# Kernel tuning notes

Measured on AMD Instinct MI355X. Metric: run time of the kernel, lower is better.

Reference implementation:

```python
import jax, jax.numpy as jnp
import numpy as np

DIM = 1024
N_HEADS = 16
HEAD_DIM = DIM // N_HEADS
WINDOW = 64


def setup_inputs() -> dict:
    key = jax.random.key(0)
    k1, k2, k3 = jax.random.split(key, 3)
    B, N = 4, 8192
    x = jax.random.normal(k1, (B, N, DIM), dtype=jnp.float32)
    w_qkv = jax.random.normal(k2, (3 * DIM, DIM), dtype=jnp.float32) * (1.0 / np.sqrt(DIM))
    b_qkv = jnp.zeros((3 * DIM,), dtype=jnp.float32)
    w_proj = jax.random.normal(k3, (DIM, DIM), dtype=jnp.float32) * (1.0 / np.sqrt(DIM))
    b_proj = jnp.zeros((DIM,), dtype=jnp.float32)
    return {"x": x, "w_qkv": w_qkv, "b_qkv": b_qkv, "w_proj": w_proj, "b_proj": b_proj}


def reference(x, w_qkv, b_qkv, w_proj, b_proj):
    B, N, C = x.shape
    H, D, W = N_HEADS, HEAD_DIM, WINDOW
    # qkv projection: torch Linear => x @ W.T + b
    qkv = x @ w_qkv.T + b_qkv                      # [B, N, 3C]
    qkv = qkv.reshape(B, N, 3, H, D).transpose(2, 0, 3, 1, 4)  # [3, B, H, N, D]
    q, k, v = qkv[0], qkv[1], qkv[2]               # each [B, H, N, D]
    n_w = N // W                                    # N chosen divisible by window
    # split sequence into non-overlapping windows (block-diagonal attention)
    qw = q.reshape(B, H, n_w, W, D)
    kw = k.reshape(B, H, n_w, W, D)
    vw = v.reshape(B, H, n_w, W, D)
    scale = 1.0 / np.sqrt(D)
    attn = jnp.einsum('bhnqd,bhnkd->bhnqk', qw, kw) * scale  # [B,H,n_w,W,W]
    attn = jax.nn.softmax(attn, axis=-1)
    out = jnp.einsum('bhnqk,bhnkd->bhnqd', attn, vw)          # [B,H,n_w,W,D]
    out = out.reshape(B, H, N, D).transpose(0, 2, 1, 3).reshape(B, N, C)
    return out @ w_proj.T + b_proj
```

## Files before the change

kernel.cpp:

```cpp
#include <hip/hip_runtime.h>
#include <hip/hip_bf16.h>
#include <cstdint>
#include <cstddef>


typedef __attribute__((ext_vector_type(8))) short short8;
typedef __attribute__((ext_vector_type(4))) float float4v;

static __device__ __forceinline__ void async16(void* lds_p, const void* g) {
  __builtin_amdgcn_global_load_lds((const __attribute__((address_space(1))) void*)g,
                                   (__attribute__((address_space(3))) void*)lds_p,
                                   16, 0, 0);
}

static __device__ __forceinline__ unsigned short f2bf_bits(float x) {
  unsigned int u = __float_as_uint(x);
  unsigned int r = (u + 0x7fffu + ((u >> 16) & 1u)) >> 16;
  return (unsigned short)r;
}

#define S_BARRIER() asm volatile("s_barrier" ::: "memory")
#define WAIT_VM(n)  asm volatile("s_waitcnt vmcnt(" #n ")" ::: "memory")
#define WAIT_LGKM0() asm volatile("s_waitcnt lgkmcnt(0)" ::: "memory")

__global__ __launch_bounds__(256) void cast_f32_to_bf16(
    const float* __restrict__ in, unsigned short* __restrict__ out, int n4) {
  int i = blockIdx.x * 256 + threadIdx.x;
  if (i >= n4) return;
  float4 v = ((const float4*)in)[i];
  ushort4 o;
  o.x = f2bf_bits(v.x); o.y = f2bf_bits(v.y);
  o.z = f2bf_bits(v.z); o.w = f2bf_bits(v.w);
  ((ushort4*)out)[i] = o;
}

template<bool OUT_BF16>
__global__ __launch_bounds__(512, 2) void gemm256(
    const unsigned short* __restrict__ A,
    const unsigned short* __restrict__ B,
    const float* __restrict__ bias,
    void* __restrict__ Cout,
    int M, int N, int K, int ntiles)
{
  extern __shared__ unsigned short lds[];

  const int t    = threadIdx.x;
  const int wave = t >> 6;
  const int lane = t & 63;
  const int lr   = lane & 15;
  const int lq   = lane >> 4;
  const int wm   = wave >> 2;
  const int wn   = wave & 3;

  const int nwg  = gridDim.x;
  const int q8   = nwg >> 3;
  const int wg   = ((int)blockIdx.x & 7) * q8 + ((int)blockIdx.x >> 3);
  const int GM   = 8;
  const int group = wg / (GM * ntiles);
  const int inG   = wg % (GM * ntiles);
  const int bm    = group * GM + (inG % GM);
  const int bn    = inG / GM;

  const int srow = t >> 3;
  const int sswz = ((t & 7) ^ (srow & 7)) << 3;
  const unsigned short* Abase = A + (size_t)(bm * 256 + srow) * K + sswz;
  const unsigned short* Bbase = B + (size_t)(bn * 256 + srow) * K + sswz;
  const int ldsw = wave * 512;

  auto stageA = [&](int kt, int c) {
    async16(lds + (kt & 1) * 16384 + c * 4096 + ldsw,
            Abase + (size_t)(c * 64) * K + kt * 64);
  };
  auto stageB = [&](int kt, int c) {
    async16(lds + 32768 + (kt & 1) * 16384 + c * 4096 + ldsw,
            Bbase + (size_t)(c * 64) * K + kt * 64);
  };

  const int g0 = ((0 + lq) ^ (lr & 7)) << 3;
  const int g1 = ((4 + lq) ^ (lr & 7)) << 3;
  const int arow0 = (wm * 128 + lr) * 64;
  const int brow0 = (wn * 64 + lr) * 64;

  float4v acc[8][4];
  #pragma unroll
  for (int i = 0; i < 8; ++i)
    #pragma unroll
    for (int j = 0; j < 4; ++j) acc[i][j] = (float4v){0.f, 0.f, 0.f, 0.f};

  const int NT = K >> 6;

  #pragma unroll
  for (int c = 0; c < 4; ++c) stageB(0, c);
  #pragma unroll
  for (int c = 0; c < 4; ++c) stageA(0, c);
  #pragma unroll
  for (int c = 0; c < 4; ++c) stageB(1, c);
  WAIT_VM(4);
  S_BARRIER();

  short8 af[4][2], bf[2][2], bf2[2][2];

  for (int kt = 0; kt < NT; ++kt) {
    const int bc = kt & 1;
    int kt1 = kt + 1; if (kt1 == NT) kt1 = 0;
    int kt2 = kt + 2; if (kt2 >= NT) kt2 -= NT;
    const unsigned short* Al = lds + bc * 16384;
    const unsigned short* Bl = lds + 32768 + bc * 16384;

    #pragma unroll
    for (int mf = 0; mf < 4; ++mf) {
      af[mf][0] = *(const short8*)(Al + arow0 + mf * 1024 + g0);
      af[mf][1] = *(const short8*)(Al + arow0 + mf * 1024 + g1);
    }
    #pragma unroll
    for (int nf = 0; nf < 2; ++nf) {
      bf[nf][0] = *(const short8*)(Bl + brow0 + nf * 1024 + g0);
      bf[nf][1] = *(const short8*)(Bl + brow0 + nf * 1024 + g1);
    }
    stageA(kt1, 0); stageA(kt1, 2);
    S_BARRIER();
    __builtin_amdgcn_s_setprio(1);
    #pragma unroll
    for (int mf = 0; mf < 4; ++mf)
      #pragma unroll
      for (int nf = 0; nf < 2; ++nf) {
        acc[mf][nf] = __builtin_amdgcn_mfma_f32_16x16x32_bf16(af[mf][0], bf[nf][0], acc[mf][nf], 0, 0, 0);
        acc[mf][nf] = __builtin_amdgcn_mfma_f32_16x16x32_bf16(af[mf][1], bf[nf][1], acc[mf][nf], 0, 0, 0);
      }
    __builtin_amdgcn_s_setprio(0);
    S_BARRIER();

    #pragma unroll
    for (int nf = 0; nf < 2; ++nf) {
      bf2[nf][0] = *(const short8*)(Bl + brow0 + (2 + nf) * 1024 + g0);
      bf2[nf][1] = *(const short8*)(Bl + brow0 + (2 + nf) * 1024 + g1);
    }
    stageA(kt1, 1); stageA(kt1, 3);
    S_BARRIER();
    __builtin_amdgcn_s_setprio(1);
    #pragma unroll
    for (int mf = 0; mf < 4; ++mf)
      #pragma unroll
      for (int nf = 0; nf < 2; ++nf) {
        acc[mf][2 + nf] = __builtin_amdgcn_mfma_f32_16x16x32_bf16(af[mf][0], bf2[nf][0], acc[mf][2 + nf], 0, 0, 0);
        acc[mf][2 + nf] = __builtin_amdgcn_mfma_f32_16x16x32_bf16(af[mf][1], bf2[nf][1], acc[mf][2 + nf], 0, 0, 0);
      }
    __builtin_amdgcn_s_setprio(0);
    S_BARRIER();

    #pragma unroll
    for (int mf = 0; mf < 4; ++mf) {
      af[mf][0] = *(const short8*)(Al + arow0 + (4 + mf) * 1024 + g0);
      af[mf][1] = *(const short8*)(Al + arow0 + (4 + mf) * 1024 + g1);
    }
    stageB(kt2, 0); stageB(kt2, 1);
    S_BARRIER();
    __builtin_amdgcn_s_setprio(1);
    #pragma unroll
    for (int mf = 0; mf < 4; ++mf)
      #pragma unroll
      for (int nf = 0; nf < 2; ++nf) {
        acc[4 + mf][nf] = __builtin_amdgcn_mfma_f32_16x16x32_bf16(af[mf][0], bf[nf][0], acc[4 + mf][nf], 0, 0, 0);
        acc[4 + mf][nf] = __builtin_amdgcn_mfma_f32_16x16x32_bf16(af[mf][1], bf[nf][1], acc[4 + mf][nf], 0, 0, 0);
      }
    __builtin_amdgcn_s_setprio(0);
    S_BARRIER();

    stageB(kt2, 2); stageB(kt2, 3);
    WAIT_VM(4);
    S_BARRIER();
    __builtin_amdgcn_s_setprio(1);
    #pragma unroll
    for (int mf = 0; mf < 4; ++mf)
      #pragma unroll
      for (int nf = 0; nf < 2; ++nf) {
        acc[4 + mf][2 + nf] = __builtin_amdgcn_mfma_f32_16x16x32_bf16(af[mf][0], bf2[nf][0], acc[4 + mf][2 + nf], 0, 0, 0);
        acc[4 + mf][2 + nf] = __builtin_amdgcn_mfma_f32_16x16x32_bf16(af[mf][1], bf2[nf][1], acc[4 + mf][2 + nf], 0, 0, 0);
      }
    __builtin_amdgcn_s_setprio(0);
    S_BARRIER();
  }

  WAIT_VM(0);

  if (OUT_BF16) {
    unsigned short* Ost = lds + wave * 4096;
    const int cb = bn * 256 + wn * 64;
    #pragma unroll
    for (int p = 0; p < 2; ++p) {
      #pragma unroll
      for (int nf = 0; nf < 4; ++nf) {
        const float bv = bias[cb + nf * 16 + lr];
        #pragma unroll
        for (int mh = 0; mh < 4; ++mh)
          #pragma unroll
          for (int r = 0; r < 4; ++r) {
            const int row = mh * 16 + lq * 4 + r;
            Ost[row * 64 + ((nf * 16 + lr) ^ (lq << 4))] =
                f2bf_bits(acc[p * 4 + mh][nf][r] + bv);
          }
      }
      #pragma unroll
      for (int k = 0; k < 8; ++k) {
        const int cid = k * 64 + lane;
        const int row = cid >> 3;
        const int c8  = cid & 7;
        const int lqr = (row >> 2) & 3;
        short8 v = *(const short8*)(Ost + row * 64 + ((c8 * 8) ^ (lqr << 4)));
        const size_t grow = (size_t)(bm * 256 + wm * 128 + p * 64 + row);
        *(short8*)((unsigned short*)Cout + grow * N + cb + c8 * 8) = v;
      }
    }
  } else {
    const int rbase = bm * 256 + wm * 128 + lq * 4;
    const int cbase = bn * 256 + wn * 64 + lr;
    #pragma unroll
    for (int nf = 0; nf < 4; ++nf) {
      const int col = cbase + nf * 16;
      const float bv = bias[col];
      #pragma unroll
      for (int mf = 0; mf < 8; ++mf) {
        const int row = rbase + mf * 16;
        #pragma unroll
        for (int r = 0; r < 4; ++r)
          ((float*)Cout)[(size_t)(row + r) * N + col] = acc[mf][nf][r] + bv;
      }
    }
  }
}

#define WPB 4

__global__ __launch_bounds__(256, 4) void win_attn(
    const unsigned short* __restrict__ qkv,
    unsigned short* __restrict__ out)
{
  __shared__ unsigned short Vt[2][64 * 64];
  __shared__ unsigned short Ps[4 * 16 * 64];

  const int t    = threadIdx.x;
  const int wave = t >> 6;
  const int lane = t & 63;
  const int lr   = lane & 15;
  const int lq   = lane >> 4;
  const int k7   = lane & 7;
  const int kh   = lane >> 3;
  const int gbase = blockIdx.x * WPB;
  unsigned short* Pst = Ps + wave * 1024;

  short8 qa[2], kf[4][2], vr[2];

  auto qptr = [&](int g) {
    const int b = g >> 11, h = (g >> 7) & 15, wi = g & 127;
    return qkv + (size_t)(b * 8192 + wi * 64) * 3072 + h * 64;
  };
  auto loadV = [&](const unsigned short* vb) {
    #pragma unroll
    for (int o = 0; o < 2; ++o)
      vr[o] = *(const short8*)(vb + (size_t)lane * 3072 + wave * 8 + o * 32);
  };
  auto loadQ = [&](const unsigned short* qb) {
    #pragma unroll
    for (int k2 = 0; k2 < 2; ++k2)
      qa[k2] = *(const short8*)(qb + (size_t)(wave * 16 + lr) * 3072 + k2 * 32 + lq * 8);
  };
  auto loadK = [&](const unsigned short* kb) {
    #pragma unroll
    for (int jt = 0; jt < 4; ++jt)
      #pragma unroll
      for (int k2 = 0; k2 < 2; ++k2)
        kf[jt][k2] = *(const short8*)(kb + (size_t)(jt * 16 + lr) * 3072 + k2 * 32 + lq * 8);
  };
  auto scatterV = [&](int s) {
    #pragma unroll
    for (int o = 0; o < 2; ++o) {
      const int d = wave * 8 + o * 32;
      #pragma unroll
      for (int j = 0; j < 8; ++j)
        Vt[s][(d + j) * 64 + k7 + ((kh ^ j) << 3)] = vr[o][j];
    }
  };

  {
    const unsigned short* qb0 = qptr(gbase);
    loadV(qb0 + 2048);
    loadK(qb0 + 1024);
    loadQ(qb0);
    scatterV(0);
    WAIT_LGKM0();
    S_BARRIER();
  }

  for (int i = 0; i < WPB; ++i) {
    const int c = i & 1;
    const int g = gbase + i;
    const int h = (g >> 7) & 15;
    const int tok0 = ((g >> 11) * 8192) + (g & 127) * 64;
    const bool more = (i + 1 < WPB);
    const unsigned short* qb1 = qptr(more ? g + 1 : g);

    if (more) loadV(qb1 + 2048);

    float4v s4[4];
    #pragma unroll
    for (int jt = 0; jt < 4; ++jt) {
      float4v a = (float4v){0.f, 0.f, 0.f, 0.f};
      #pragma unroll
      for (int k2 = 0; k2 < 2; ++k2)
        a = __builtin_amdgcn_mfma_f32_16x16x32_bf16(qa[k2], kf[jt][k2], a, 0, 0, 0);
      s4[jt] = a;
    }

    if (more) { loadK(qb1 + 1024); loadQ(qb1); }

    const float scale = 0.125f;
    float pr[4][4];
    #pragma unroll
    for (int r = 0; r < 4; ++r) {
      float m = s4[0][r];
      #pragma unroll
      for (int jt = 1; jt < 4; ++jt) m = fmaxf(m, s4[jt][r]);
      #pragma unroll
      for (int off = 1; off < 16; off <<= 1) m = fmaxf(m, __shfl_xor(m, off));
      float sum = 0.f;
      #pragma unroll
      for (int jt = 0; jt < 4; ++jt) {
        float e = __expf((s4[jt][r] - m) * scale);
        pr[jt][r] = e; sum += e;
      }
      #pragma unroll
      for (int off = 1; off < 16; off <<= 1) sum += __shfl_xor(sum, off);
      float inv = 1.0f / sum;
      #pragma unroll
      for (int jt = 0; jt < 4; ++jt) pr[jt][r] *= inv;
    }

    #pragma unroll
    for (int jt = 0; jt < 4; ++jt)
      #pragma unroll
      for (int r = 0; r < 4; ++r) {
        const int row = lq * 4 + r;
        const int cu  = (jt * 2 + (lr >> 3)) ^ (row & 7);
        Pst[row * 64 + (cu << 3) + (lr & 7)] = f2bf_bits(pr[jt][r]);
      }
    short8 pa[2];
    #pragma unroll
    for (int k2 = 0; k2 < 2; ++k2)
      pa[k2] = *(const short8*)(&Pst[lr * 64 + (((k2 * 4 + lq) ^ (lr & 7)) << 3)]);

    float4v o4[4];
    #pragma unroll
    for (int jd = 0; jd < 4; ++jd) {
      float4v a = (float4v){0.f, 0.f, 0.f, 0.f};
      #pragma unroll
      for (int k2 = 0; k2 < 2; ++k2) {
        short8 vf = *(const short8*)(&Vt[c][(jd * 16 + lr) * 64 +
                                            (((k2 * 4 + lq) ^ (lr & 7)) << 3)]);
        a = __builtin_amdgcn_mfma_f32_16x16x32_bf16(pa[k2], vf, a, 0, 0, 0);
      }
      o4[jd] = a;
    }

    if (more) scatterV(c ^ 1);

    #pragma unroll
    for (int jd = 0; jd < 4; ++jd)
      #pragma unroll
      for (int r = 0; r < 4; ++r)
        Pst[(lq * 4 + r) * 64 + ((jd * 16 + lr) ^ (lq << 4))] = f2bf_bits(o4[jd][r]);
    #pragma unroll
    for (int k = 0; k < 2; ++k) {
      const int cid = k * 64 + lane;
      const int row = cid >> 3;
      const int c8  = cid & 7;
      const int lqr = (row >> 2) & 3;
      short8 v = *(const short8*)(&Pst[row * 64 + ((c8 * 8) ^ (lqr << 4))]);
      *(short8*)(out + (size_t)(tok0 + wave * 16 + row) * 1024 + h * 64 + c8 * 8) = v;
    }

    if (more) {
      WAIT_LGKM0();
      S_BARRIER();
    }
  }
}

extern "C" void kernel_launch(void* const* d_in, const int* in_sizes, int n_in,
                              void* d_out, int out_size, void* d_ws, size_t ws_size,
                              hipStream_t stream) {
  const float* x      = (const float*)d_in[0];
  const float* w_qkv  = (const float*)d_in[1];
  const float* b_qkv  = (const float*)d_in[2];
  const float* w_proj = (const float*)d_in[3];
  const float* b_proj = (const float*)d_in[4];
  float* outp = (float*)d_out;

  char* ws = (char*)d_ws;
  unsigned short* xb     = (unsigned short*)(ws);
  unsigned short* wqkvb  = (unsigned short*)(ws + 67108864);
  unsigned short* wprojb = (unsigned short*)(ws + 73400320);
  unsigned short* qkvb   = (unsigned short*)(ws + 75497472);
  unsigned short* attnb  = (unsigned short*)(ws + 276824064);

  static int attr_done = 0;
  if (!attr_done) {
    hipFuncSetAttribute(reinterpret_cast<const void*>(&gemm256<true>),
                        hipFuncAttributeMaxDynamicSharedMemorySize, 131072);
    hipFuncSetAttribute(reinterpret_cast<const void*>(&gemm256<false>),
                        hipFuncAttributeMaxDynamicSharedMemorySize, 131072);
    attr_done = 1;
  }

  cast_f32_to_bf16<<<32768, 256, 0, stream>>>(x,      xb,     33554432 / 4);
  cast_f32_to_bf16<<<3072,  256, 0, stream>>>(w_qkv,  wqkvb,  3145728 / 4);
  cast_f32_to_bf16<<<1024,  256, 0, stream>>>(w_proj, wprojb, 1048576 / 4);

  gemm256<true><<<128 * 12, 512, 131072, stream>>>(xb, wqkvb, b_qkv, qkvb,
                                                   32768, 3072, 1024, 12);
  win_attn<<<8192 / WPB, 256, 0, stream>>>(qkvb, attnb);
  gemm256<false><<<128 * 4, 512, 131072, stream>>>(attnb, wprojb, b_proj, outp,
                                                   32768, 1024, 1024, 4);
}
```

Before: 589.9 us.

## Assign one attention window per wave instead of block-shared windows

The windowed attention kernel now gives each wave a whole (batch, head, window) tile. Each wave loads K and V, computes all four 16-row query tiles, and transposes V through its own LDS slice. The block barriers and the cross-wave double-buffered V scatter go away, as does the software prefetch of the next window. In exchange, per-wave LDS use and register pressure rise (pa, vf and vrow are held together), and loads are no longer overlapped with compute across windows.

```diff
diff --git a/kernel.cpp b/kernel.cpp
--- a/kernel.cpp
+++ b/kernel.cpp
@@ -21,7 +21,6 @@
 
 #define S_BARRIER() asm volatile("s_barrier" ::: "memory")
 #define WAIT_VM(n)  asm volatile("s_waitcnt vmcnt(" #n ")" ::: "memory")
-#define WAIT_LGKM0() asm volatile("s_waitcnt lgkmcnt(0)" ::: "memory")
 
 __global__ __launch_bounds__(256) void cast_f32_to_bf16(
     const float* __restrict__ in, unsigned short* __restrict__ out, int n4) {
@@ -229,77 +228,48 @@
   }
 }
 
-#define WPB 4
-
 __global__ __launch_bounds__(256, 4) void win_attn(
     const unsigned short* __restrict__ qkv,
     unsigned short* __restrict__ out)
 {
-  __shared__ unsigned short Vt[2][64 * 64];
-  __shared__ unsigned short Ps[4 * 16 * 64];
+  __shared__ unsigned short Ps[4][64 * 64];
 
   const int t    = threadIdx.x;
   const int wave = t >> 6;
   const int lane = t & 63;
   const int lr   = lane & 15;
   const int lq   = lane >> 4;
+  const int kh   = lane >> 3;
   const int k7   = lane & 7;
-  const int kh   = lane >> 3;
-  const int gbase = blockIdx.x * WPB;
-  unsigned short* Pst = Ps + wave * 1024;
-
-  short8 qa[2], kf[4][2], vr[2];
-
-  auto qptr = [&](int g) {
-    const int b = g >> 11, h = (g >> 7) & 15, wi = g & 127;
-    return qkv + (size_t)(b * 8192 + wi * 64) * 3072 + h * 64;
-  };
-  auto loadV = [&](const unsigned short* vb) {
-    #pragma unroll
-    for (int o = 0; o < 2; ++o)
-      vr[o] = *(const short8*)(vb + (size_t)lane * 3072 + wave * 8 + o * 32);
-  };
-  auto loadQ = [&](const unsigned short* qb) {
+
+  const int g    = blockIdx.x * 4 + wave;
+  const int h    = (g >> 7) & 15;
+  const int tok0 = ((g >> 11) * 8192) + (g & 127) * 64;
+  const unsigned short* qb = qkv + (size_t)tok0 * 3072 + h * 64;
+  const unsigned short* kb = qb + 1024;
+  const unsigned short* vb = qb + 2048;
+  unsigned short* Pst = Ps[wave];
+
+  short8 kf[4][2];
+  #pragma unroll
+  for (int jt = 0; jt < 4; ++jt)
     #pragma unroll
     for (int k2 = 0; k2 < 2; ++k2)
-      qa[k2] = *(const short8*)(qb + (size_t)(wave * 16 + lr) * 3072 + k2 * 32 + lq * 8);
-  };
-  auto loadK = [&](const unsigned short* kb) {
-    #pragma unroll
-    for (int jt = 0; jt < 4; ++jt)
-      #pragma unroll
-      for (int k2 = 0; k2 < 2; ++k2)
-        kf[jt][k2] = *(const short8*)(kb + (size_t)(jt * 16 + lr) * 3072 + k2 * 32 + lq * 8);
-  };
-  auto scatterV = [&](int s) {
-    #pragma unroll
-    for (int o = 0; o < 2; ++o) {
-      const int d = wave * 8 + o * 32;
-      #pragma unroll
-      for (int j = 0; j < 8; ++j)
-        Vt[s][(d + j) * 64 + k7 + ((kh ^ j) << 3)] = vr[o][j];
-    }
-  };
-
-  {
-    const unsigned short* qb0 = qptr(gbase);
-    loadV(qb0 + 2048);
-    loadK(qb0 + 1024);
-    loadQ(qb0);
-    scatterV(0);
-    WAIT_LGKM0();
-    S_BARRIER();
-  }
-
-  for (int i = 0; i < WPB; ++i) {
-    const int c = i & 1;
-    const int g = gbase + i;
-    const int h = (g >> 7) & 15;
-    const int tok0 = ((g >> 11) * 8192) + (g & 127) * 64;
-    const bool more = (i + 1 < WPB);
-    const unsigned short* qb1 = qptr(more ? g + 1 : g);
-
-    if (more) loadV(qb1 + 2048);
+      kf[jt][k2] = *(const short8*)(kb + (size_t)(jt * 16 + lr) * 3072 + k2 * 32 + lq * 8);
+
+  short8 vrow[8];
+  #pragma unroll
+  for (int o = 0; o < 8; ++o)
+    vrow[o] = *(const short8*)(vb + (size_t)lane * 3072 + o * 8);
+
+  const float scale = 0.125f;
+
+  #pragma unroll
+  for (int mt = 0; mt < 4; ++mt) {
+    short8 qa[2];
+    #pragma unroll
+    for (int k2 = 0; k2 < 2; ++k2)
+      qa[k2] = *(const short8*)(qb + (size_t)(mt * 16 + lr) * 3072 + k2 * 32 + lq * 8);
 
     float4v s4[4];
     #pragma unroll
@@ -311,10 +281,6 @@
       s4[jt] = a;
     }
 
-    if (more) { loadK(qb1 + 1024); loadQ(qb1); }
-
-    const float scale = 0.125f;
-    float pr[4][4];
     #pragma unroll
     for (int r = 0; r < 4; ++r) {
       float m = s4[0][r];
@@ -323,65 +289,69 @@
       #pragma unroll
       for (int off = 1; off < 16; off <<= 1) m = fmaxf(m, __shfl_xor(m, off));
       float sum = 0.f;
+      float pr[4];
       #pragma unroll
       for (int jt = 0; jt < 4; ++jt) {
         float e = __expf((s4[jt][r] - m) * scale);
-        pr[jt][r] = e; sum += e;
+        pr[jt] = e; sum += e;
       }
       #pragma unroll
       for (int off = 1; off < 16; off <<= 1) sum += __shfl_xor(sum, off);
       float inv = 1.0f / sum;
-      #pragma unroll
-      for (int jt = 0; jt < 4; ++jt) pr[jt][r] *= inv;
-    }
-
-    #pragma unroll
-    for (int jt = 0; jt < 4; ++jt)
-      #pragma unroll
-      for (int r = 0; r < 4; ++r) {
-        const int row = lq * 4 + r;
-        const int cu  = (jt * 2 + (lr >> 3)) ^ (row & 7);
-        Pst[row * 64 + (cu << 3) + (lr & 7)] = f2bf_bits(pr[jt][r]);
-      }
-    short8 pa[2];
+      const int row = mt * 16 + lq * 4 + r;
+      #pragma unroll
+      for (int jt = 0; jt < 4; ++jt) {
+        const int cu = (jt * 2 + (lr >> 3)) ^ (row & 7);
+        Pst[row * 64 + (cu << 3) + (lr & 7)] = f2bf_bits(pr[jt] * inv);
+      }
+    }
+  }
+
+  short8 pa[4][2];
+  #pragma unroll
+  for (int mt = 0; mt < 4; ++mt)
     #pragma unroll
     for (int k2 = 0; k2 < 2; ++k2)
-      pa[k2] = *(const short8*)(&Pst[lr * 64 + (((k2 * 4 + lq) ^ (lr & 7)) << 3)]);
-
-    float4v o4[4];
+      pa[mt][k2] = *(const short8*)(&Pst[(mt * 16 + lr) * 64 +
+                                         (((k2 * 4 + lq) ^ (lr & 7)) << 3)]);
+
+  #pragma unroll
+  for (int o = 0; o < 8; ++o)
+    #pragma unroll
+    for (int j = 0; j < 8; ++j)
+      Pst[(o * 8 + j) * 64 + ((kh ^ j) << 3) + k7] = vrow[o][j];
+
+  short8 vf[4][2];
+  #pragma unroll
+  for (int jd = 0; jd < 4; ++jd)
+    #pragma unroll
+    for (int k2 = 0; k2 < 2; ++k2)
+      vf[jd][k2] = *(const short8*)(&Pst[(jd * 16 + lr) * 64 +
+                                         (((k2 * 4 + lq) ^ (lr & 7)) << 3)]);
+
+  #pragma unroll
+  for (int mt = 0; mt < 4; ++mt)
     #pragma unroll
     for (int jd = 0; jd < 4; ++jd) {
       float4v a = (float4v){0.f, 0.f, 0.f, 0.f};
       #pragma unroll
-      for (int k2 = 0; k2 < 2; ++k2) {
-        short8 vf = *(const short8*)(&Vt[c][(jd * 16 + lr) * 64 +
-                                            (((k2 * 4 + lq) ^ (lr & 7)) << 3)]);
-        a = __builtin_amdgcn_mfma_f32_16x16x32_bf16(pa[k2], vf, a, 0, 0, 0);
-      }
-      o4[jd] = a;
-    }
-
-    if (more) scatterV(c ^ 1);
-
-    #pragma unroll
-    for (int jd = 0; jd < 4; ++jd)
-      #pragma unroll
-      for (int r = 0; r < 4; ++r)
-        Pst[(lq * 4 + r) * 64 + ((jd * 16 + lr) ^ (lq << 4))] = f2bf_bits(o4[jd][r]);
-    #pragma unroll
-    for (int k = 0; k < 2; ++k) {
-      const int cid = k * 64 + lane;
-      const int row = cid >> 3;
-      const int c8  = cid & 7;
-      const int lqr = (row >> 2) & 3;
-      short8 v = *(const short8*)(&Pst[row * 64 + ((c8 * 8) ^ (lqr << 4))]);
-      *(short8*)(out + (size_t)(tok0 + wave * 16 + row) * 1024 + h * 64 + c8 * 8) = v;
-    }
-
-    if (more) {
-      WAIT_LGKM0();
-      S_BARRIER();
-    }
+      for (int k2 = 0; k2 < 2; ++k2)
+        a = __builtin_amdgcn_mfma_f32_16x16x32_bf16(pa[mt][k2], vf[jd][k2], a, 0, 0, 0);
+      #pragma unroll
+      for (int r = 0; r < 4; ++r) {
+        const int row = mt * 16 + lq * 4 + r;
+        Pst[row * 64 + ((jd * 16 + lr) ^ (lq << 4))] = f2bf_bits(a[r]);
+      }
+    }
+
+  #pragma unroll
+  for (int k = 0; k < 8; ++k) {
+    const int cid = k * 64 + lane;
+    const int row = cid >> 3;
+    const int c8  = cid & 7;
+    const int lqr = (row >> 2) & 3;
+    short8 v = *(const short8*)(&Pst[row * 64 + ((c8 * 8) ^ (lqr << 4))]);
+    *(short8*)(out + (size_t)(tok0 + row) * 1024 + h * 64 + c8 * 8) = v;
   }
 }
 
@@ -417,7 +387,7 @@
 
   gemm256<true><<<128 * 12, 512, 131072, stream>>>(xb, wqkvb, b_qkv, qkvb,
                                                    32768, 3072, 1024, 12);
-  win_attn<<<8192 / WPB, 256, 0, stream>>>(qkvb, attnb);
+  win_attn<<<8192 / 4, 256, 0, stream>>>(qkvb, attnb);
   gemm256<false><<<128 * 4, 512, 131072, stream>>>(attnb, wprojb, b_proj, outp,
                                                    32768, 1024, 1024, 4);
 }
```

New measurement: 579.9 us. No clear change (-1.7%).
